# Optimization experiments

Hardware: AMD Instinct MI355X
Metric: run time of the kernel (lower is better)

Reference implementation:

```python
import jax, jax.numpy as jnp
import numpy as np

N_NODES = 100000
D = 256
N_TYPES = 4
E1 = 300000
E2 = 300000


def setup_inputs() -> dict:
    key = jax.random.key(0)
    ks = jax.random.split(key, 9)
    x = jax.random.normal(ks[0], (N_NODES, D), dtype=jnp.float32)
    hyperedge_index_s1 = jax.random.randint(ks[1], (2, E1 * 1), 0, N_NODES, dtype=jnp.int32)
    hyperedge_type_s1 = jax.random.randint(ks[2], (E1,), 0, N_TYPES, dtype=jnp.int32)
    hyperedge_index_s2 = jax.random.randint(ks[3], (2, E2 * 2), 0, N_NODES, dtype=jnp.int32)
    hyperedge_type_s2 = jax.random.randint(ks[4], (E2,), 0, N_TYPES, dtype=jnp.int32)
    # xavier_normal init for A: std = sqrt(2 / (fan_in + fan_out))
    A_s1 = jax.random.normal(ks[5], (N_TYPES, 1 * D, D), dtype=jnp.float32) * np.sqrt(2.0 / (D + D)).astype(np.float32)
    A_s2 = jax.random.normal(ks[6], (N_TYPES, 2 * D, D), dtype=jnp.float32) * np.sqrt(2.0 / (2 * D + D)).astype(np.float32)
    lim = 1.0 / np.sqrt(D)
    W_c = jax.random.uniform(ks[7], (D, D), minval=-lim, maxval=lim, dtype=jnp.float32)
    b_c = jax.random.uniform(ks[8], (D,), minval=-lim, maxval=lim, dtype=jnp.float32)
    return dict(x=x,
                hyperedge_index_s1=hyperedge_index_s1, hyperedge_type_s1=hyperedge_type_s1,
                hyperedge_index_s2=hyperedge_index_s2, hyperedge_type_s2=hyperedge_type_s2,
                A_s1=A_s1, A_s2=A_s2, W_c=W_c, b_c=b_c)


def _shape_agg(x, A, idx, etype, shape, n_nodes):
    """Per-hyperedge-shape gather -> per-type matmul -> normalize -> scatter-add."""
    d = x.shape[1]
    e = etype.shape[0]
    # concat the `shape` source node features per hyperedge: [E, shape*d]
    src = x[idx[0]].reshape(e, shape * d)
    # first target slot per hyperedge: [E]
    dst = idx[1].reshape(e, shape)[:, 0]
    agg = jnp.zeros((n_nodes, d), dtype=x.dtype)
    for t in range(A.shape[0]):  # small fixed number of edge types
        mask = etype == t
        tmp = src @ A[t]  # [E, d]
        # per-destination count within this (shape, type) group == torch.unique counts
        counts = jax.ops.segment_sum(mask.astype(x.dtype), dst, num_segments=n_nodes)
        norm = jnp.where(mask, 1.0 / jnp.maximum(counts[dst], 1.0), 0.0)
        agg = agg.at[dst].add(norm[:, None] * tmp)
    return agg


def reference(x, hyperedge_index_s1, hyperedge_type_s1,
              hyperedge_index_s2, hyperedge_type_s2,
              A_s1, A_s2, W_c, b_c):
    n = x.shape[0]
    agg = _shape_agg(x, A_s1, hyperedge_index_s1, hyperedge_type_s1, 1, n)
    agg = agg + _shape_agg(x, A_s2, hyperedge_index_s2, hyperedge_type_s2, 2, n)
    return x @ W_c.T + b_c + agg
```

## Files before the change

### kernel.cpp

```cpp
#include <hip/hip_runtime.h>
#include <stdint.h>

#define N_NODES 100000
#define D 256
#define NT 4

typedef float f32x4 __attribute__((ext_vector_type(4)));
typedef __bf16 bf16x8 __attribute__((ext_vector_type(8)));
typedef unsigned int uint32x4 __attribute__((ext_vector_type(4)));
typedef unsigned int uint32x2 __attribute__((ext_vector_type(2)));

__device__ __forceinline__ unsigned short f2bf(float f) {
    unsigned u = __float_as_uint(f);
    u += 0x7FFF + ((u >> 16) & 1);
    return (unsigned short)(u >> 16);
}

__device__ __forceinline__ void gload_lds16(const void* g, void* lds) {
    __builtin_amdgcn_global_load_lds(
        (const __attribute__((address_space(1))) unsigned int*)g,
        (__attribute__((address_space(3))) unsigned int*)lds, 16, 0, 0);
}


template<int SHAPE>
__global__ void k_count(const int* __restrict__ idx, const int* __restrict__ etype,
                        int E, int* __restrict__ counts) {
    int e = blockIdx.x * 256 + threadIdx.x;
    if (e >= E) return;
    int t = etype[e];
    int dst = idx[(size_t)SHAPE * E + (size_t)SHAPE * e];
    atomicAdd(&counts[t * N_NODES + dst], 1);
}


__global__ __launch_bounds__(256) void k_scan1(const int* __restrict__ in, int n,
        int* __restrict__ outv, int* __restrict__ bsums) {
    __shared__ int s[256];
    int tid = threadIdx.x;
    int i = blockIdx.x * 1024 + tid * 4;
    int v0 = 0, v1 = 0, v2 = 0, v3 = 0;
    if (i + 3 < n) {
        int4 v = *(const int4*)(in + i);
        v0 = v.x; v1 = v.y; v2 = v.z; v3 = v.w;
    } else {
        if (i     < n) v0 = in[i];
        if (i + 1 < n) v1 = in[i + 1];
        if (i + 2 < n) v2 = in[i + 2];
        if (i + 3 < n) v3 = in[i + 3];
    }
    int tsum = v0 + v1 + v2 + v3;
    s[tid] = tsum; __syncthreads();
    for (int off = 1; off < 256; off <<= 1) {
        int t = (tid >= off) ? s[tid - off] : 0;
        __syncthreads();
        s[tid] += t;
        __syncthreads();
    }
    int excl = s[tid] - tsum;
    if (tid == 255) bsums[blockIdx.x] = s[255];
    int o0 = excl, o1 = o0 + v0, o2 = o1 + v1, o3 = o2 + v2;
    if (i + 3 < n) {
        *(int4*)(outv + i) = make_int4(o0, o1, o2, o3);
    } else {
        if (i     < n) outv[i]     = o0;
        if (i + 1 < n) outv[i + 1] = o1;
        if (i + 2 < n) outv[i + 2] = o2;
        if (i + 3 < n) outv[i + 3] = o3;
    }
}

__global__ void k_scan2(int* __restrict__ bsums, int nb) {
    __shared__ int s[512];
    int t = threadIdx.x;
    int v = (t < nb) ? bsums[t] : 0;
    s[t] = v; __syncthreads();
    for (int off = 1; off < 512; off <<= 1) {
        int u = (t >= off) ? s[t - off] : 0;
        __syncthreads();
        s[t] += u;
        __syncthreads();
    }
    if (t < nb) bsums[t] = s[t] - v;
}

__global__ __launch_bounds__(256) void k_scan3(int* __restrict__ cellofs,
        int* __restrict__ cellcur, const int* __restrict__ bsums, int n) {
    int i = blockIdx.x * 1024 + threadIdx.x * 4;
    int add = bsums[blockIdx.x];
    if (i + 3 < n) {
        int4 v = *(int4*)(cellofs + i);
        v.x += add; v.y += add; v.z += add; v.w += add;
        *(int4*)(cellofs + i) = v;
        *(int4*)(cellcur + i) = v;
    } else {
        for (int k = 0; k < 4; ++k)
            if (i + k < n) { int v = cellofs[i + k] + add; cellofs[i + k] = v; cellcur[i + k] = v; }
    }
}


template<int SHAPE>
__global__ void k_place(const int* __restrict__ idx, const int* __restrict__ etype, int E,
                        int* __restrict__ cellcur, int* __restrict__ bucket) {
    int e = blockIdx.x * 256 + threadIdx.x;
    if (e >= E) return;
    int t = etype[e];
    int dst = idx[(size_t)SHAPE * E + (size_t)SHAPE * e];
    int pos = atomicAdd(&cellcur[t * N_NODES + dst], 1);
    bucket[pos] = e;
}


__global__ __launch_bounds__(256) void k_cvt(const float* __restrict__ in,
        unsigned short* __restrict__ ob, int n8) {
    int i = blockIdx.x * 256 + threadIdx.x;
    if (i >= n8) return;
    const float4* p = (const float4*)in + (size_t)i * 2;
    float4 v0 = p[0], v1 = p[1];
    union { unsigned short us[8]; uint4 u4; } o;
    o.us[0] = f2bf(v0.x); o.us[1] = f2bf(v0.y); o.us[2] = f2bf(v0.z); o.us[3] = f2bf(v0.w);
    o.us[4] = f2bf(v1.x); o.us[5] = f2bf(v1.y); o.us[6] = f2bf(v1.z); o.us[7] = f2bf(v1.w);
    *(uint4*)(ob + (size_t)i * 8) = o.u4;
}


__global__ void k_cvt_At(const float* __restrict__ A, unsigned short* __restrict__ AT, int K) {
    __shared__ float tl[32][33];
    const float* Ab = A + (size_t)blockIdx.z * K * D;
    unsigned short* Ob = AT + (size_t)blockIdx.z * D * K;
    int k0 = blockIdx.x * 32, j0 = blockIdx.y * 32;
    int lx = threadIdx.x, ly = threadIdx.y;
    for (int yy = ly; yy < 32; yy += 8)
        tl[yy][lx] = Ab[(size_t)(k0 + yy) * D + j0 + lx];
    __syncthreads();
    for (int yy = ly; yy < 32; yy += 8)
        Ob[(size_t)(j0 + yy) * K + k0 + lx] = f2bf(tl[lx][yy]);
}


__global__ __launch_bounds__(256) void k_init_mfma(const unsigned short* __restrict__ xb,
        const unsigned short* __restrict__ Wb, const float* __restrict__ bias,
        float* __restrict__ out, int n) {
    __shared__ __align__(16) char xs[64 * 128];
    int row0 = blockIdx.x * 64;
    int tid = threadIdx.x;
    int lane = tid & 63, w = tid >> 6;
    int l15 = lane & 15, l4 = lane >> 4;
    f32x4 acc[4][4];
    #pragma unroll
    for (int m = 0; m < 4; ++m)
        #pragma unroll
        for (int nn = 0; nn < 4; ++nn) acc[m][nn] = (f32x4)0.f;

    for (int kk = 0; kk < D; kk += 64) {
        #pragma unroll
        for (int it = 0; it < 2; ++it) {
            int f = it * 256 + tid;
            int r = f >> 3, q0 = f & 7;
            int q = q0 ^ (r & 7);
            int gr = row0 + r; if (gr >= n) gr = n - 1;
            gload_lds16(xb + (size_t)gr * D + kk + q * 8, xs + f * 16);
        }
        bf16x8 bfr[2][4];
        #pragma unroll
        for (int ks = 0; ks < 2; ++ks)
            #pragma unroll
            for (int nn = 0; nn < 4; ++nn) {
                int j = w * 64 + nn * 16 + l15;
                int k = kk + ks * 32 + l4 * 8;
                bfr[ks][nn] = *(const bf16x8*)(Wb + (size_t)j * D + k);
            }
        __syncthreads();
        #pragma unroll
        for (int ks = 0; ks < 2; ++ks)
            #pragma unroll
            for (int m = 0; m < 4; ++m) {
                int R = m * 16 + l15;
                int C = ks * 4 + l4;
                bf16x8 a = *(const bf16x8*)(xs + R * 128 + ((C ^ (R & 7)) << 4));
                #pragma unroll
                for (int nn = 0; nn < 4; ++nn)
                    acc[m][nn] = __builtin_amdgcn_mfma_f32_16x16x32_bf16(
                        a, bfr[ks][nn], acc[m][nn], 0, 0, 0);
            }
        __syncthreads();
    }
    #pragma unroll
    for (int m = 0; m < 4; ++m)
        #pragma unroll
        for (int nn = 0; nn < 4; ++nn) {
            int col = w * 64 + nn * 16 + l15;
            float bv = bias[col];
            #pragma unroll
            for (int r = 0; r < 4; ++r) {
                int row = row0 + m * 16 + l4 * 4 + r;
                if (row < n) out[(size_t)row * D + col] = acc[m][nn][r] + bv;
            }
        }
}


template<int SHAPE, int SCR>
__global__ __launch_bounds__(256, 4) void k_edge_mfma(const unsigned short* __restrict__ xb,
        const int* __restrict__ idx, const unsigned short* __restrict__ AT,
        float* __restrict__ out, unsigned short* __restrict__ eo, int E,
        const int* __restrict__ counts, const int* __restrict__ cellofs,
        const int* __restrict__ bucket) {
    constexpr int K = SHAPE * 256;
    __shared__ __align__(16) char smem[16 * 264 * 2];
    __shared__ int srcS[SHAPE][64];
    __shared__ int dstS[64];
    __shared__ float normS[64];

    int t = blockIdx.y;
    int offs_t = cellofs[t * N_NODES];
    int end_t = (t == NT - 1) ? E : cellofs[(t + 1) * N_NODES];
    int cnt = end_t - offs_t;
    int tile = blockIdx.x * 64;
    if (tile >= cnt) return;
    int nE = min(64, cnt - tile);
    int base = offs_t + tile;
    int tid = threadIdx.x;

    if (tid < 64) {
        bool valid = tid < nE;
        int e = bucket[base + (valid ? tid : 0)];
        int dst = idx[(size_t)SHAPE * E + (size_t)SHAPE * e];
        dstS[tid] = dst;
        int c = counts[t * N_NODES + dst];
        normS[tid] = valid ? 1.0f / (float)(c > 1 ? c : 1) : 0.0f;
        srcS[0][tid] = idx[SHAPE * e];
        if (SHAPE == 2) srcS[SHAPE - 1][tid] = idx[SHAPE * e + SHAPE - 1];
    }
    __syncthreads();

    const unsigned short* Bt = AT + (size_t)t * D * K;
    int lane = tid & 63, w = tid >> 6;
    int l15 = lane & 15, l4 = lane >> 4;
    f32x4 acc[4][4];
    #pragma unroll
    for (int m = 0; m < 4; ++m)
        #pragma unroll
        for (int nn = 0; nn < 4; ++nn) acc[m][nn] = (f32x4)0.f;

    for (int kk = 0; kk < K; kk += 64) {
        #pragma unroll
        for (int it = 0; it < 2; ++it) {
            int f = it * 256 + tid;
            int r = f >> 3, q0 = f & 7;
            int q = q0 ^ (r & 7);
            int node = srcS[SHAPE == 2 ? (kk >> 8) : 0][r];
            int col = (kk & 255) + q * 8;
            gload_lds16(xb + (size_t)node * D + col, smem + f * 16);
        }
        bf16x8 bfr[2][4];
        #pragma unroll
        for (int ks = 0; ks < 2; ++ks)
            #pragma unroll
            for (int nn = 0; nn < 4; ++nn) {
                int j = w * 64 + nn * 16 + l15;
                int k = kk + ks * 32 + l4 * 8;
                bfr[ks][nn] = *(const bf16x8*)(Bt + (size_t)j * K + k);
            }
        __syncthreads();
        #pragma unroll
        for (int ks = 0; ks < 2; ++ks)
            #pragma unroll
            for (int m = 0; m < 4; ++m) {
                int R = m * 16 + l15;
                int C = ks * 4 + l4;
                bf16x8 a = *(const bf16x8*)(smem + R * 128 + ((C ^ (R & 7)) << 4));
                #pragma unroll
                for (int nn = 0; nn < 4; ++nn)
                    acc[m][nn] = __builtin_amdgcn_mfma_f32_16x16x32_bf16(
                        a, bfr[ks][nn], acc[m][nn], 0, 0, 0);
            }
        __syncthreads();
    }

    if constexpr (SCR) {
        unsigned short (*re)[264] = (unsigned short (*)[264])smem;
        #pragma unroll
        for (int q = 0; q < 4; ++q) {
            if (q) __syncthreads();
            #pragma unroll
            for (int r = 0; r < 4; ++r) {
                int rl = l4 * 4 + r;
                float nm = normS[q * 16 + rl];
                #pragma unroll
                for (int nn = 0; nn < 4; ++nn) {
                    int col = w * 64 + nn * 16 + l15;
                    re[rl][col] = f2bf(nm * acc[q][nn][r]);
                }
            }
            __syncthreads();
            #pragma unroll
            for (int it = 0; it < 2; ++it) {
                int f = it * 256 + tid;
                int row = f >> 5, seg = f & 31;
                int grow = q * 16 + row;
                if (grow < nE) {
                    uint32x4 v = *(const uint32x4*)&re[row][seg * 8];
                    *(uint32x4*)(eo + (size_t)(base + grow) * D + seg * 8) = v;
                }
            }
        }
    } else {
        #pragma unroll
        for (int m = 0; m < 4; ++m)
            #pragma unroll
            for (int r = 0; r < 4; ++r) {
                int rr = m * 16 + l4 * 4 + r;
                if (rr < nE) {
                    float nm = normS[rr];
                    size_t ob = (size_t)dstS[rr] * D;
                    #pragma unroll
                    for (int nn = 0; nn < 4; ++nn) {
                        int col = w * 64 + nn * 16 + l15;
                        atomicAdd(&out[ob + col], nm * acc[m][nn][r]);
                    }
                }
            }
    }
}


__device__ __forceinline__ void acc_runs(const unsigned short* __restrict__ eo,
        const int* __restrict__ counts, const int* __restrict__ cellofs,
        int dst, int lane, float& a0, float& a1, float& a2, float& a3, int& tot) {
    #pragma unroll
    for (int t = 0; t < NT; ++t) {
        int start = cellofs[t * N_NODES + dst];
        int c = counts[t * N_NODES + dst];
        tot += c;
        for (int i = 0; i < c; ++i) {
            const uint32x2* row = (const uint32x2*)(eo + (size_t)(start + i) * D + lane * 4);
            uint32x2 v = __builtin_nontemporal_load(row);
            a0 += __uint_as_float(v.x << 16);
            a1 += __uint_as_float(v.x & 0xFFFF0000u);
            a2 += __uint_as_float(v.y << 16);
            a3 += __uint_as_float(v.y & 0xFFFF0000u);
        }
    }
}

__global__ __launch_bounds__(256) void k_reduce_one(const unsigned short* __restrict__ eo,
        const int* __restrict__ counts, const int* __restrict__ cellofs,
        float* __restrict__ out) {
    int wv = threadIdx.x >> 6, lane = threadIdx.x & 63;
    int dst = blockIdx.x * 4 + wv;
    if (dst >= N_NODES) return;
    float a0 = 0.f, a1 = 0.f, a2 = 0.f, a3 = 0.f;
    int tot = 0;
    acc_runs(eo, counts, cellofs, dst, lane, a0, a1, a2, a3, tot);
    if (tot) {
        float4* o = (float4*)&out[(size_t)dst * D + lane * 4];
        float4 cur = *o;
        cur.x += a0; cur.y += a1; cur.z += a2; cur.w += a3;
        *o = cur;
    }
}

__global__ __launch_bounds__(256) void k_reduce_two(
        const unsigned short* __restrict__ eo1, const int* __restrict__ c1, const int* __restrict__ o1,
        const unsigned short* __restrict__ eo2, const int* __restrict__ c2, const int* __restrict__ o2,
        float* __restrict__ out) {
    int wv = threadIdx.x >> 6, lane = threadIdx.x & 63;
    int dst = blockIdx.x * 4 + wv;
    if (dst >= N_NODES) return;
    float a0 = 0.f, a1 = 0.f, a2 = 0.f, a3 = 0.f;
    int tot = 0;
    acc_runs(eo1, c1, o1, dst, lane, a0, a1, a2, a3, tot);
    acc_runs(eo2, c2, o2, dst, lane, a0, a1, a2, a3, tot);
    if (tot) {
        float4* o = (float4*)&out[(size_t)dst * D + lane * 4];
        float4 cur = *o;
        cur.x += a0; cur.y += a1; cur.z += a2; cur.w += a3;
        *o = cur;
    }
}


extern "C" void kernel_launch(void* const* d_in, const int* in_sizes, int n_in,
                              void* d_out, int out_size, void* d_ws, size_t ws_size,
                              hipStream_t stream) {
    const float* x  = (const float*)d_in[0];
    const int* idx1 = (const int*)d_in[1];
    const int* ty1  = (const int*)d_in[2];
    const int* idx2 = (const int*)d_in[3];
    const int* ty2  = (const int*)d_in[4];
    const float* A1 = (const float*)d_in[5];
    const float* A2 = (const float*)d_in[6];
    const float* W  = (const float*)d_in[7];
    const float* b  = (const float*)d_in[8];
    float* out = (float*)d_out;

    int E1 = in_sizes[2];
    int E2 = in_sizes[4];
    int maxE = E1 > E2 ? E1 : E2;
    const int NCELL = NT * N_NODES;
    const int NB = (NCELL + 1023) / 1024;
    const int NRB = (N_NODES + 3) / 4;

    char* p = (char*)d_ws;
    unsigned short* xb  = (unsigned short*)p; p += (size_t)N_NODES * D * 2;
    unsigned short* Wb  = (unsigned short*)p; p += (size_t)D * D * 2;
    unsigned short* A1T = (unsigned short*)p; p += (size_t)NT * D * 256 * 2;
    unsigned short* A2T = (unsigned short*)p; p += (size_t)NT * D * 512 * 2;
    int* counts1 = (int*)p; p += (size_t)NCELL * 4;
    int* cellofs1= (int*)p; p += (size_t)NCELL * 4;
    int* counts2 = (int*)p; p += (size_t)NCELL * 4;
    int* cellofs2= (int*)p; p += (size_t)NCELL * 4;
    int* cellcur = (int*)p; p += (size_t)NCELL * 4;
    int* bsums   = (int*)p; p += 512 * 4;
    int* bucket  = (int*)p; p += (size_t)maxE * 4;
    unsigned short* eo1 = (unsigned short*)p; p += (size_t)maxE * D * 2;
    size_t need1 = (size_t)(p - (char*)d_ws);
    unsigned short* eo2 = (unsigned short*)p; p += (size_t)maxE * D * 2;
    size_t need2 = (size_t)(p - (char*)d_ws);
    int mode = (need2 <= ws_size) ? 2 : (need1 <= ws_size) ? 1 : 0;

    k_cvt<<<(N_NODES * D / 8 + 255) / 256, 256, 0, stream>>>(x, xb, N_NODES * D / 8);
    k_cvt<<<(D * D / 8 + 255) / 256, 256, 0, stream>>>(W, Wb, D * D / 8);
    k_cvt_At<<<dim3(256 / 32, D / 32, NT), dim3(32, 8), 0, stream>>>(A1, A1T, 256);
    k_cvt_At<<<dim3(512 / 32, D / 32, NT), dim3(32, 8), 0, stream>>>(A2, A2T, 512);

    k_init_mfma<<<(N_NODES + 63) / 64, 256, 0, stream>>>(xb, Wb, b, out, N_NODES);

    hipMemsetAsync(counts1, 0, (size_t)NCELL * sizeof(int), stream);
    k_count<1><<<(E1 + 255) / 256, 256, 0, stream>>>(idx1, ty1, E1, counts1);
    k_scan1<<<NB, 256, 0, stream>>>(counts1, NCELL, cellofs1, bsums);
    k_scan2<<<1, 512, 0, stream>>>(bsums, NB);
    k_scan3<<<NB, 256, 0, stream>>>(cellofs1, cellcur, bsums, NCELL);
    k_place<1><<<(E1 + 255) / 256, 256, 0, stream>>>(idx1, ty1, E1, cellcur, bucket);
    if (mode) {
        k_edge_mfma<1, 1><<<dim3((E1 + 63) / 64, NT), 256, 0, stream>>>(
            xb, idx1, A1T, out, eo1, E1, counts1, cellofs1, bucket);
        if (mode == 1)
            k_reduce_one<<<NRB, 256, 0, stream>>>(eo1, counts1, cellofs1, out);
    } else {
        k_edge_mfma<1, 0><<<dim3((E1 + 63) / 64, NT), 256, 0, stream>>>(
            xb, idx1, A1T, out, nullptr, E1, counts1, cellofs1, bucket);
    }

    hipMemsetAsync(counts2, 0, (size_t)NCELL * sizeof(int), stream);
    k_count<2><<<(E2 + 255) / 256, 256, 0, stream>>>(idx2, ty2, E2, counts2);
    k_scan1<<<NB, 256, 0, stream>>>(counts2, NCELL, cellofs2, bsums);
    k_scan2<<<1, 512, 0, stream>>>(bsums, NB);
    k_scan3<<<NB, 256, 0, stream>>>(cellofs2, cellcur, bsums, NCELL);
    k_place<2><<<(E2 + 255) / 256, 256, 0, stream>>>(idx2, ty2, E2, cellcur, bucket);
    if (mode) {
        unsigned short* eoS2 = (mode == 2) ? eo2 : eo1;
        k_edge_mfma<2, 1><<<dim3((E2 + 63) / 64, NT), 256, 0, stream>>>(
            xb, idx2, A2T, out, eoS2, E2, counts2, cellofs2, bucket);
        if (mode == 2)
            k_reduce_two<<<NRB, 256, 0, stream>>>(eo1, counts1, cellofs1,
                                                  eo2, counts2, cellofs2, out);
        else
            k_reduce_one<<<NRB, 256, 0, stream>>>(eo1, counts2, cellofs2, out);
    } else {
        k_edge_mfma<2, 0><<<dim3((E2 + 63) / 64, NT), 256, 0, stream>>>(
            xb, idx2, A2T, out, nullptr, E2, counts2, cellofs2, bucket);
    }
}
```

Measured before the change: 588.4 us.

## Load gathered A fragments directly from global into registers, dropping LDS staging

```diff
diff --git a/kernel.cpp b/kernel.cpp
--- a/kernel.cpp
+++ b/kernel.cpp
@@ -208,7 +208,7 @@
         const int* __restrict__ counts, const int* __restrict__ cellofs,
         const int* __restrict__ bucket) {
     constexpr int K = SHAPE * 256;
-    __shared__ __align__(16) char smem[16 * 264 * 2];
+    __shared__ __align__(16) unsigned short re[16][264];
     __shared__ int srcS[SHAPE][64];
     __shared__ int dstS[64];
     __shared__ float normS[64];
@@ -238,22 +238,34 @@
     const unsigned short* Bt = AT + (size_t)t * D * K;
     int lane = tid & 63, w = tid >> 6;
     int l15 = lane & 15, l4 = lane >> 4;
+
+    const unsigned short* rowp[SHAPE][4];
+    #pragma unroll
+    for (int m = 0; m < 4; ++m) {
+        rowp[0][m] = xb + (size_t)srcS[0][m * 16 + l15] * D;
+        if (SHAPE == 2)
+            rowp[SHAPE - 1][m] = xb + (size_t)srcS[SHAPE - 1][m * 16 + l15] * D;
+    }
+
     f32x4 acc[4][4];
     #pragma unroll
     for (int m = 0; m < 4; ++m)
         #pragma unroll
         for (int nn = 0; nn < 4; ++nn) acc[m][nn] = (f32x4)0.f;
 
-    for (int kk = 0; kk < K; kk += 64) {
-        #pragma unroll
-        for (int it = 0; it < 2; ++it) {
-            int f = it * 256 + tid;
-            int r = f >> 3, q0 = f & 7;
-            int q = q0 ^ (r & 7);
-            int node = srcS[SHAPE == 2 ? (kk >> 8) : 0][r];
-            int col = (kk & 255) + q * 8;
-            gload_lds16(xb + (size_t)node * D + col, smem + f * 16);
-        }
+    #pragma unroll
+    for (int st = 0; st < K / 64; ++st) {
+        constexpr int SB = 1;
+        int kk = st * 64;
+        int bank = (SHAPE == 2) ? (st >> 2) : 0;
+        int col0 = kk & 255;
+        (void)SB;
+        bf16x8 afr[2][4];
+        #pragma unroll
+        for (int ks = 0; ks < 2; ++ks)
+            #pragma unroll
+            for (int m = 0; m < 4; ++m)
+                afr[ks][m] = *(const bf16x8*)(rowp[bank][m] + col0 + (ks * 4 + l4) * 8);
         bf16x8 bfr[2][4];
         #pragma unroll
         for (int ks = 0; ks < 2; ++ks)
@@ -263,27 +275,20 @@
                 int k = kk + ks * 32 + l4 * 8;
                 bfr[ks][nn] = *(const bf16x8*)(Bt + (size_t)j * K + k);
             }
-        __syncthreads();
         #pragma unroll
         for (int ks = 0; ks < 2; ++ks)
             #pragma unroll
-            for (int m = 0; m < 4; ++m) {
-                int R = m * 16 + l15;
-                int C = ks * 4 + l4;
-                bf16x8 a = *(const bf16x8*)(smem + R * 128 + ((C ^ (R & 7)) << 4));
+            for (int m = 0; m < 4; ++m)
                 #pragma unroll
                 for (int nn = 0; nn < 4; ++nn)
                     acc[m][nn] = __builtin_amdgcn_mfma_f32_16x16x32_bf16(
-                        a, bfr[ks][nn], acc[m][nn], 0, 0, 0);
-            }
-        __syncthreads();
+                        afr[ks][m], bfr[ks][nn], acc[m][nn], 0, 0, 0);
     }
 
     if constexpr (SCR) {
-        unsigned short (*re)[264] = (unsigned short (*)[264])smem;
         #pragma unroll
         for (int q = 0; q < 4; ++q) {
-            if (q) __syncthreads();
+            __syncthreads();
             #pragma unroll
             for (int r = 0; r < 4; ++r) {
                 int rl = l4 * 4 + r;
```

After: 793.6 us. +34.9%, slower.

## Double-buffer gathered edge rows in LDS with register prefetch

Applied to the files above, without the earlier changes.

```diff
diff --git a/kernel.cpp b/kernel.cpp
--- a/kernel.cpp
+++ b/kernel.cpp
@@ -208,7 +208,8 @@
         const int* __restrict__ counts, const int* __restrict__ cellofs,
         const int* __restrict__ bucket) {
     constexpr int K = SHAPE * 256;
-    __shared__ __align__(16) char smem[16 * 264 * 2];
+    constexpr int NST = K / 64;
+    __shared__ __align__(16) char smem[2 * 64 * 128];
     __shared__ int srcS[SHAPE][64];
     __shared__ int dstS[64];
     __shared__ float normS[64];
@@ -238,21 +239,43 @@
     const unsigned short* Bt = AT + (size_t)t * D * K;
     int lane = tid & 63, w = tid >> 6;
     int l15 = lane & 15, l4 = lane >> 4;
+
+    int f0 = tid, f1 = 256 + tid;
+    int r0 = f0 >> 3, gq0 = (((f0 & 7) ^ (r0 & 7)) << 4);
+    int r1 = f1 >> 3, gq1 = (((f1 & 7) ^ (r1 & 7)) << 4);
+
+    const char* pA0 = (const char*)(xb + (size_t)srcS[0][r0] * D);
+    const char* pA1 = (const char*)(xb + (size_t)srcS[0][r1] * D);
+    const char* pB0 = pA0;
+    const char* pB1 = pA1;
+    if constexpr (SHAPE == 2) {
+        pB0 = (const char*)(xb + (size_t)srcS[1][r0] * D);
+        pB1 = (const char*)(xb + (size_t)srcS[1][r1] * D);
+    }
+
     f32x4 acc[4][4];
     #pragma unroll
     for (int m = 0; m < 4; ++m)
         #pragma unroll
         for (int nn = 0; nn < 4; ++nn) acc[m][nn] = (f32x4)0.f;
 
-    for (int kk = 0; kk < K; kk += 64) {
-        #pragma unroll
-        for (int it = 0; it < 2; ++it) {
-            int f = it * 256 + tid;
-            int r = f >> 3, q0 = f & 7;
-            int q = q0 ^ (r & 7);
-            int node = srcS[SHAPE == 2 ? (kk >> 8) : 0][r];
-            int col = (kk & 255) + q * 8;
-            gload_lds16(xb + (size_t)node * D + col, smem + f * 16);
+    uint32x4 s0 = *(const uint32x4*)(pA0 + gq0);
+    uint32x4 s1 = *(const uint32x4*)(pA1 + gq1);
+
+    #pragma unroll
+    for (int st = 0; st < NST; ++st) {
+        char* buf = smem + (st & 1) * 8192;
+        int kk = st * 64;
+        *(uint32x4*)(buf + f0 * 16) = s0;
+        *(uint32x4*)(buf + f1 * 16) = s1;
+        if (st + 1 < NST) {
+            int sn = st + 1;
+            int colB = ((sn * 64) & 255) * 2;
+            const char* b0 = pA0;
+            const char* b1 = pA1;
+            if constexpr (SHAPE == 2) { if (sn >= 4) { b0 = pB0; b1 = pB1; } }
+            s0 = *(const uint32x4*)(b0 + colB + gq0);
+            s1 = *(const uint32x4*)(b1 + colB + gq1);
         }
         bf16x8 bfr[2][4];
         #pragma unroll
@@ -270,20 +293,19 @@
             for (int m = 0; m < 4; ++m) {
                 int R = m * 16 + l15;
                 int C = ks * 4 + l4;
-                bf16x8 a = *(const bf16x8*)(smem + R * 128 + ((C ^ (R & 7)) << 4));
+                bf16x8 a = *(const bf16x8*)(buf + R * 128 + ((C ^ (R & 7)) << 4));
                 #pragma unroll
                 for (int nn = 0; nn < 4; ++nn)
                     acc[m][nn] = __builtin_amdgcn_mfma_f32_16x16x32_bf16(
                         a, bfr[ks][nn], acc[m][nn], 0, 0, 0);
             }
-        __syncthreads();
     }
 
     if constexpr (SCR) {
         unsigned short (*re)[264] = (unsigned short (*)[264])smem;
         #pragma unroll
         for (int q = 0; q < 4; ++q) {
-            if (q) __syncthreads();
+            __syncthreads();
             #pragma unroll
             for (int r = 0; r < 4; ++r) {
                 int rl = l4 * 4 + r;
```

Result: slower. 641.8 us (+9.1%).

## Merge bucketing passes for both hyperedge shapes into one count/scan/place pipeline

Applied to the files above, without the earlier changes.

```diff
diff --git a/kernel.cpp b/kernel.cpp
--- a/kernel.cpp
+++ b/kernel.cpp
@@ -23,14 +23,20 @@
 }
 
 
-template<int SHAPE>
-__global__ void k_count(const int* __restrict__ idx, const int* __restrict__ etype,
-                        int E, int* __restrict__ counts) {
+__global__ void k_count_both(const int* __restrict__ idx1, const int* __restrict__ ty1, int E1,
+                             const int* __restrict__ idx2, const int* __restrict__ ty2, int E2,
+                             int* __restrict__ counts) {
     int e = blockIdx.x * 256 + threadIdx.x;
-    if (e >= E) return;
-    int t = etype[e];
-    int dst = idx[(size_t)SHAPE * E + (size_t)SHAPE * e];
-    atomicAdd(&counts[t * N_NODES + dst], 1);
+    if (e < E1) {
+        int t = ty1[e];
+        int dst = idx1[(size_t)E1 + e];
+        atomicAdd(&counts[t * N_NODES + dst], 1);
+    }
+    if (e < E2) {
+        int t = ty2[e];
+        int dst = idx2[(size_t)2 * E2 + (size_t)2 * e];
+        atomicAdd(&counts[NT * N_NODES + t * N_NODES + dst], 1);
+    }
 }
 
 
@@ -70,12 +76,12 @@
     }
 }
 
-__global__ void k_scan2(int* __restrict__ bsums, int nb) {
-    __shared__ int s[512];
+__global__ __launch_bounds__(1024) void k_scan2(int* __restrict__ bsums, int nb) {
+    __shared__ int s[1024];
     int t = threadIdx.x;
     int v = (t < nb) ? bsums[t] : 0;
     s[t] = v; __syncthreads();
-    for (int off = 1; off < 512; off <<= 1) {
+    for (int off = 1; off < 1024; off <<= 1) {
         int u = (t >= off) ? s[t - off] : 0;
         __syncthreads();
         s[t] += u;
@@ -100,15 +106,24 @@
 }
 
 
-template<int SHAPE>
-__global__ void k_place(const int* __restrict__ idx, const int* __restrict__ etype, int E,
-                        int* __restrict__ cellcur, int* __restrict__ bucket) {
+__global__ void k_place_both(const int* __restrict__ idx1, const int* __restrict__ ty1, int E1,
+                             int* __restrict__ bucket1,
+                             const int* __restrict__ idx2, const int* __restrict__ ty2, int E2,
+                             int* __restrict__ bucket2,
+                             int* __restrict__ cellcur) {
     int e = blockIdx.x * 256 + threadIdx.x;
-    if (e >= E) return;
-    int t = etype[e];
-    int dst = idx[(size_t)SHAPE * E + (size_t)SHAPE * e];
-    int pos = atomicAdd(&cellcur[t * N_NODES + dst], 1);
-    bucket[pos] = e;
+    if (e < E1) {
+        int t = ty1[e];
+        int dst = idx1[(size_t)E1 + e];
+        int pos = atomicAdd(&cellcur[t * N_NODES + dst], 1);
+        bucket1[pos] = e;
+    }
+    if (e < E2) {
+        int t = ty2[e];
+        int dst = idx2[(size_t)2 * E2 + (size_t)2 * e];
+        int pos = atomicAdd(&cellcur[NT * N_NODES + t * N_NODES + dst], 1) - E1;
+        bucket2[pos] = e;
+    }
 }
 
 
@@ -204,18 +219,19 @@
 template<int SHAPE, int SCR>
 __global__ __launch_bounds__(256, 4) void k_edge_mfma(const unsigned short* __restrict__ xb,
         const int* __restrict__ idx, const unsigned short* __restrict__ AT,
-        float* __restrict__ out, unsigned short* __restrict__ eo, int E,
+        float* __restrict__ out, unsigned short* __restrict__ eo, int E, int rebase,
         const int* __restrict__ counts, const int* __restrict__ cellofs,
         const int* __restrict__ bucket) {
     constexpr int K = SHAPE * 256;
-    __shared__ __align__(16) char smem[16 * 264 * 2];
+    __shared__ __align__(16) unsigned short re[16][264];
+    __shared__ __align__(16) char xs[64 * 128];
     __shared__ int srcS[SHAPE][64];
     __shared__ int dstS[64];
     __shared__ float normS[64];
 
     int t = blockIdx.y;
-    int offs_t = cellofs[t * N_NODES];
-    int end_t = (t == NT - 1) ? E : cellofs[(t + 1) * N_NODES];
+    int offs_t = cellofs[t * N_NODES] - rebase;
+    int end_t = (t == NT - 1) ? E : cellofs[(t + 1) * N_NODES] - rebase;
     int cnt = end_t - offs_t;
     int tile = blockIdx.x * 64;
     if (tile >= cnt) return;
@@ -252,7 +268,7 @@
             int q = q0 ^ (r & 7);
             int node = srcS[SHAPE == 2 ? (kk >> 8) : 0][r];
             int col = (kk & 255) + q * 8;
-            gload_lds16(xb + (size_t)node * D + col, smem + f * 16);
+            gload_lds16(xb + (size_t)node * D + col, xs + f * 16);
         }
         bf16x8 bfr[2][4];
         #pragma unroll
@@ -270,7 +286,7 @@
             for (int m = 0; m < 4; ++m) {
                 int R = m * 16 + l15;
                 int C = ks * 4 + l4;
-                bf16x8 a = *(const bf16x8*)(smem + R * 128 + ((C ^ (R & 7)) << 4));
+                bf16x8 a = *(const bf16x8*)(xs + R * 128 + ((C ^ (R & 7)) << 4));
                 #pragma unroll
                 for (int nn = 0; nn < 4; ++nn)
                     acc[m][nn] = __builtin_amdgcn_mfma_f32_16x16x32_bf16(
@@ -280,10 +296,9 @@
     }
 
     if constexpr (SCR) {
-        unsigned short (*re)[264] = (unsigned short (*)[264])smem;
         #pragma unroll
         for (int q = 0; q < 4; ++q) {
-            if (q) __syncthreads();
+            __syncthreads();
             #pragma unroll
             for (int r = 0; r < 4; ++r) {
                 int rl = l4 * 4 + r;
@@ -327,11 +342,11 @@
 
 
 __device__ __forceinline__ void acc_runs(const unsigned short* __restrict__ eo,
-        const int* __restrict__ counts, const int* __restrict__ cellofs,
+        const int* __restrict__ counts, const int* __restrict__ cellofs, int rebase,
         int dst, int lane, float& a0, float& a1, float& a2, float& a3, int& tot) {
     #pragma unroll
     for (int t = 0; t < NT; ++t) {
-        int start = cellofs[t * N_NODES + dst];
+        int start = cellofs[t * N_NODES + dst] - rebase;
         int c = counts[t * N_NODES + dst];
         tot += c;
         for (int i = 0; i < c; ++i) {
@@ -346,14 +361,14 @@
 }
 
 __global__ __launch_bounds__(256) void k_reduce_one(const unsigned short* __restrict__ eo,
-        const int* __restrict__ counts, const int* __restrict__ cellofs,
+        const int* __restrict__ counts, const int* __restrict__ cellofs, int rebase,
         float* __restrict__ out) {
     int wv = threadIdx.x >> 6, lane = threadIdx.x & 63;
     int dst = blockIdx.x * 4 + wv;
     if (dst >= N_NODES) return;
     float a0 = 0.f, a1 = 0.f, a2 = 0.f, a3 = 0.f;
     int tot = 0;
-    acc_runs(eo, counts, cellofs, dst, lane, a0, a1, a2, a3, tot);
+    acc_runs(eo, counts, cellofs, rebase, dst, lane, a0, a1, a2, a3, tot);
     if (tot) {
         float4* o = (float4*)&out[(size_t)dst * D + lane * 4];
         float4 cur = *o;
@@ -363,16 +378,18 @@
 }
 
 __global__ __launch_bounds__(256) void k_reduce_two(
-        const unsigned short* __restrict__ eo1, const int* __restrict__ c1, const int* __restrict__ o1,
-        const unsigned short* __restrict__ eo2, const int* __restrict__ c2, const int* __restrict__ o2,
+        const unsigned short* __restrict__ eo1, const int* __restrict__ c1,
+        const int* __restrict__ o1,
+        const unsigned short* __restrict__ eo2, const int* __restrict__ c2,
+        const int* __restrict__ o2, int rb2,
         float* __restrict__ out) {
     int wv = threadIdx.x >> 6, lane = threadIdx.x & 63;
     int dst = blockIdx.x * 4 + wv;
     if (dst >= N_NODES) return;
     float a0 = 0.f, a1 = 0.f, a2 = 0.f, a3 = 0.f;
     int tot = 0;
-    acc_runs(eo1, c1, o1, dst, lane, a0, a1, a2, a3, tot);
-    acc_runs(eo2, c2, o2, dst, lane, a0, a1, a2, a3, tot);
+    acc_runs(eo1, c1, o1, 0, dst, lane, a0, a1, a2, a3, tot);
+    acc_runs(eo2, c2, o2, rb2, dst, lane, a0, a1, a2, a3, tot);
     if (tot) {
         float4* o = (float4*)&out[(size_t)dst * D + lane * 4];
         float4 cur = *o;
@@ -400,7 +417,8 @@
     int E2 = in_sizes[4];
     int maxE = E1 > E2 ? E1 : E2;
     const int NCELL = NT * N_NODES;
-    const int NB = (NCELL + 1023) / 1024;
+    const int NC2 = 2 * NCELL;
+    const int NB2 = (NC2 + 1023) / 1024;
     const int NRB = (N_NODES + 3) / 4;
 
     char* p = (char*)d_ws;
@@ -408,18 +426,18 @@
     unsigned short* Wb  = (unsigned short*)p; p += (size_t)D * D * 2;
     unsigned short* A1T = (unsigned short*)p; p += (size_t)NT * D * 256 * 2;
     unsigned short* A2T = (unsigned short*)p; p += (size_t)NT * D * 512 * 2;
-    int* counts1 = (int*)p; p += (size_t)NCELL * 4;
-    int* cellofs1= (int*)p; p += (size_t)NCELL * 4;
-    int* counts2 = (int*)p; p += (size_t)NCELL * 4;
-    int* cellofs2= (int*)p; p += (size_t)NCELL * 4;
-    int* cellcur = (int*)p; p += (size_t)NCELL * 4;
-    int* bsums   = (int*)p; p += 512 * 4;
-    int* bucket  = (int*)p; p += (size_t)maxE * 4;
+    int* counts  = (int*)p; p += (size_t)NC2 * 4;
+    int* cellofs = (int*)p; p += (size_t)NC2 * 4;
+    int* cellcur = (int*)p; p += (size_t)NC2 * 4;
+    int* bsums   = (int*)p; p += 1024 * 4;
+    int* bucket1 = (int*)p; p += (size_t)maxE * 4;
+    int* bucket2 = (int*)p; p += (size_t)maxE * 4;
     unsigned short* eo1 = (unsigned short*)p; p += (size_t)maxE * D * 2;
-    size_t need1 = (size_t)(p - (char*)d_ws);
     unsigned short* eo2 = (unsigned short*)p; p += (size_t)maxE * D * 2;
     size_t need2 = (size_t)(p - (char*)d_ws);
-    int mode = (need2 <= ws_size) ? 2 : (need1 <= ws_size) ? 1 : 0;
+    int mode = (need2 <= ws_size) ? 2 : 0;
+    int* counts2  = counts + NCELL;
+    int* cellofs2 = cellofs + NCELL;
 
     k_cvt<<<(N_NODES * D / 8 + 255) / 256, 256, 0, stream>>>(x, xb, N_NODES * D / 8);
     k_cvt<<<(D * D / 8 + 255) / 256, 256, 0, stream>>>(W, Wb, D * D / 8);
@@ -428,39 +446,25 @@
 
     k_init_mfma<<<(N_NODES + 63) / 64, 256, 0, stream>>>(xb, Wb, b, out, N_NODES);
 
-    hipMemsetAsync(counts1, 0, (size_t)NCELL * sizeof(int), stream);
-    k_count<1><<<(E1 + 255) / 256, 256, 0, stream>>>(idx1, ty1, E1, counts1);
-    k_scan1<<<NB, 256, 0, stream>>>(counts1, NCELL, cellofs1, bsums);
-    k_scan2<<<1, 512, 0, stream>>>(bsums, NB);
-    k_scan3<<<NB, 256, 0, stream>>>(cellofs1, cellcur, bsums, NCELL);
-    k_place<1><<<(E1 + 255) / 256, 256, 0, stream>>>(idx1, ty1, E1, cellcur, bucket);
-    if (mode) {
+    hipMemsetAsync(counts, 0, (size_t)NC2 * sizeof(int), stream);
+    k_count_both<<<(maxE + 255) / 256, 256, 0, stream>>>(idx1, ty1, E1, idx2, ty2, E2, counts);
+    k_scan1<<<NB2, 256, 0, stream>>>(counts, NC2, cellofs, bsums);
+    k_scan2<<<1, 1024, 0, stream>>>(bsums, NB2);
+    k_scan3<<<NB2, 256, 0, stream>>>(cellofs, cellcur, bsums, NC2);
+    k_place_both<<<(maxE + 255) / 256, 256, 0, stream>>>(idx1, ty1, E1, bucket1,
+                                                          idx2, ty2, E2, bucket2, cellcur);
+
+    if (mode == 2) {
         k_edge_mfma<1, 1><<<dim3((E1 + 63) / 64, NT), 256, 0, stream>>>(
-            xb, idx1, A1T, out, eo1, E1, counts1, cellofs1, bucket);
-        if (mode == 1)
-            k_reduce_one<<<NRB, 256, 0, stream>>>(eo1, counts1, cellofs1, out);
+            xb, idx1, A1T, out, eo1, E1, 0, counts, cellofs, bucket1);
+        k_edge_mfma<2, 1><<<dim3((E2 + 63) / 64, NT), 256, 0, stream>>>(
+            xb, idx2, A2T, out, eo2, E2, E1, counts2, cellofs2, bucket2);
+        k_reduce_two<<<NRB, 256, 0, stream>>>(eo1, counts, cellofs,
+                                              eo2, counts2, cellofs2, E1, out);
     } else {
         k_edge_mfma<1, 0><<<dim3((E1 + 63) / 64, NT), 256, 0, stream>>>(
-            xb, idx1, A1T, out, nullptr, E1, counts1, cellofs1, bucket);
-    }
-
-    hipMemsetAsync(counts2, 0, (size_t)NCELL * sizeof(int), stream);
-    k_count<2><<<(E2 + 255) / 256, 256, 0, stream>>>(idx2, ty2, E2, counts2);
-    k_scan1<<<NB, 256, 0, stream>>>(counts2, NCELL, cellofs2, bsums);
-    k_scan2<<<1, 512, 0, stream>>>(bsums, NB);
-    k_scan3<<<NB, 256, 0, stream>>>(cellofs2, cellcur, bsums, NCELL);
-    k_place<2><<<(E2 + 255) / 256, 256, 0, stream>>>(idx2, ty2, E2, cellcur, bucket);
-    if (mode) {
-        unsigned short* eoS2 = (mode == 2) ? eo2 : eo1;
-        k_edge_mfma<2, 1><<<dim3((E2 + 63) / 64, NT), 256, 0, stream>>>(
-            xb, idx2, A2T, out, eoS2, E2, counts2, cellofs2, bucket);
-        if (mode == 2)
-            k_reduce_two<<<NRB, 256, 0, stream>>>(eo1, counts1, cellofs1,
-                                                  eo2, counts2, cellofs2, out);
-        else
-            k_reduce_one<<<NRB, 256, 0, stream>>>(eo1, counts2, cellofs2, out);
-    } else {
+            xb, idx1, A1T, out, nullptr, E1, 0, counts, cellofs, bucket1);
         k_edge_mfma<2, 0><<<dim3((E2 + 63) / 64, NT), 256, 0, stream>>>(
-            xb, idx2, A2T, out, nullptr, E2, counts2, cellofs2, bucket);
-    }
-}
+            xb, idx2, A2T, out, nullptr, E2, E1, counts2, cellofs2, bucket2);
+    }
+}
```

After: 573.7 us. -2.5%, faster.
